# Optimization experiments

Hardware: AMD Instinct MI355X
Metric: run time of the kernel (lower is better)

## Reference

```python
import jax, jax.numpy as jnp
import numpy as np

SQRT_D_K = 64 ** 0.5  # d_model ** 0.5 from __init__
NEG_INF = -1e9


def setup_inputs() -> dict:
    key = jax.random.key(0)
    kq, kk, kv, kp = jax.random.split(key, 4)
    B, H, S, Dh = 4, 16, 2048, 64
    q = jax.random.normal(kq, (B, H, S, Dh), dtype=jnp.float32)
    k = jax.random.normal(kk, (B, H, S, Dh), dtype=jnp.float32)
    v = jax.random.normal(kv, (B, H, S, Dh), dtype=jnp.float32)
    # causal mask: 1 above the diagonal (positions to mask), [1,1,S,S]
    casual_mask = jnp.triu(jnp.ones((S, S), dtype=jnp.int32), k=1)[None, None]
    # padding mask: 1 marks padded tokens, [B,S]
    padding_mask = jax.random.randint(kp, (B, S), 0, 2, dtype=jnp.int32)
    return {"q": q, "k": k, "v": v, "casual_mask": casual_mask,
            "padding_mask": padding_mask}


def reference(q, k, v, casual_mask, padding_mask):
    # score: [B,H,S,S]
    score = jnp.einsum("bhqd,bhkd->bhqk", q, k) / SQRT_D_K
    score = jnp.where(casual_mask == 1, NEG_INF, score)
    score = jnp.where(padding_mask[:, None, None, :] == 1, NEG_INF, score)
    attn_weights = jax.nn.softmax(score, axis=-1)
    # dropout p=0.0 (eval) -> identity
    attention_output = jnp.einsum("bhqk,bhkd->bhqd", attn_weights, v)
    return attention_output, attn_weights
```

## Files before the change

### kernel.cpp

```cpp
#include <hip/hip_runtime.h>
#include <hip/hip_bf16.h>

#define S_LEN 2048
#define DH    64
#define QT    128
#define KT    64
#define NW    4

typedef __attribute__((ext_vector_type(8))) short bf16x8;
typedef __attribute__((ext_vector_type(4))) float f32x4;
typedef __attribute__((ext_vector_type(4))) unsigned u32x4;
typedef __attribute__((ext_vector_type(2))) unsigned u32x2;

static __device__ __forceinline__ unsigned cvtpk(float a, float b) {
    unsigned r;
    asm("v_cvt_pk_bf16_f32 %0, %1, %2" : "=v"(r) : "v"(a), "v"(b));
    return r;
}

__global__ __launch_bounds__(256) void attn_main(
    const float* __restrict__ Q, const float* __restrict__ K,
    const float* __restrict__ V, const int* __restrict__ PAD,
    float* __restrict__ OUT, float* __restrict__ W)
{
    __shared__ short Kt[KT][72];
    __shared__ short VT[DH][72];
    __shared__ short Pb[NW][16][72];
    __shared__ float sinv[2][NW][16];
    __shared__ unsigned long long padm[32];

    const int orig = blockIdx.x;
    const int wg   = (orig & 7) * 128 + (orig >> 3);
    const int bh   = wg >> 4;
    const int qt   = 15 - (wg & 15);
    const int b    = bh >> 4;
    const int q0   = qt * QT;

    const int tid  = threadIdx.x;
    const int wv   = tid >> 6;
    const int l    = tid & 63;
    const int lr   = l & 15;
    const int lg   = l >> 4;
    const int k2   = (tid & 31) * 2;
    const int dblk = (tid >> 5) * 8;

    const size_t hoff = (size_t)bh * S_LEN * DH;
    const float* Qh = Q + hoff;
    const float* Kh = K + hoff;
    const float* Vh = V + hoff;
    float* Oh = OUT + hoff;
    float* Wh = W + (size_t)bh * S_LEN * S_LEN;

    const int nkt    = 2 * qt + 2;
    const int ktmaxA = 2 * qt;

    for (int i = tid; i < S_LEN; i += 256) {
        unsigned long long m = __ballot(PAD[b * S_LEN + i] != 0);
        if (l == 0) padm[i >> 6] = m;
    }

    bf16x8 qfA[2], qfB[2];
    #pragma unroll
    for (int blk = 0; blk < 2; ++blk) {
        const float* qp = Qh + (size_t)(q0 + blk * 64 + wv * 16 + lr) * DH + lg * 8;
        #pragma unroll
        for (int h = 0; h < 2; ++h) {
            f32x4 a  = *reinterpret_cast<const f32x4*>(qp + h * 32);
            f32x4 b4 = *reinterpret_cast<const f32x4*>(qp + h * 32 + 4);
            u32x4 t;
            t[0] = cvtpk(a[0] * 0.125f,  a[1] * 0.125f);
            t[1] = cvtpk(a[2] * 0.125f,  a[3] * 0.125f);
            t[2] = cvtpk(b4[0] * 0.125f, b4[1] * 0.125f);
            t[3] = cvtpk(b4[2] * 0.125f, b4[3] * 0.125f);
            (blk ? qfB[h] : qfA[h]) = __builtin_bit_cast(bf16x8, t);
        }
    }

    const f32x4 z4 = {0.f, 0.f, 0.f, 0.f};
    f32x4 accA[4] = {z4, z4, z4, z4};
    f32x4 accB[4] = {z4, z4, z4, z4};
    float rsA = 0.f, rsB = 0.f;
    const int qcolA = q0 + wv * 16 + lr;
    const int qcolB = qcolA + 64;

    auto ablock = [&](const bf16x8 (&qf)[2], const int qcol, float& rsref,
                      f32x4 (&accb)[4], const unsigned long long pm, const int ktbase) {
        f32x4 sc[4] = {z4, z4, z4, z4};
        #pragma unroll
        for (int s = 0; s < 4; ++s)
            #pragma unroll
            for (int h = 0; h < 2; ++h) {
                bf16x8 kf = *reinterpret_cast<const bf16x8*>(&Kt[s * 16 + lr][h * 32 + lg * 8]);
                sc[s] = __builtin_amdgcn_mfma_f32_16x16x32_bf16(kf, qf[h], sc[s], 0, 0, 0);
            }
        #pragma unroll
        for (int s = 0; s < 4; ++s) {
            const int kbase = ktbase + s * 16 + lg * 4;
            float e[4];
            #pragma unroll
            for (int r = 0; r < 4; ++r) {
                const bool padded = (pm >> (s * 16 + lg * 4 + r)) & 1ull;
                const bool ok = (kbase + r <= qcol) && !padded;
                e[r] = ok ? __expf(sc[s][r]) : 0.f;
                rsref += e[r];
            }
            u32x2 p2 = { cvtpk(e[0], e[1]), cvtpk(e[2], e[3]) };
            *reinterpret_cast<u32x2*>(&Pb[wv][lr][s * 16 + lg * 4]) = p2;
        }
        #pragma unroll
        for (int kk = 0; kk < 2; ++kk) {
            bf16x8 pf = *reinterpret_cast<const bf16x8*>(&Pb[wv][lr][kk * 32 + lg * 8]);
            #pragma unroll
            for (int dt = 0; dt < 4; ++dt) {
                bf16x8 vf = *reinterpret_cast<const bf16x8*>(&VT[dt * 16 + lr][kk * 32 + lg * 8]);
                accb[dt] = __builtin_amdgcn_mfma_f32_16x16x32_bf16(pf, vf, accb[dt], 0, 0, 0);
            }
        }
    };

    for (int kt = 0; kt < nkt; ++kt) {
        __syncthreads();
        {
            const float* kp = Kh + ((size_t)(kt * KT) + l) * DH + wv * 16;
            f32x4 pk0 = *reinterpret_cast<const f32x4*>(kp);
            f32x4 pk1 = *reinterpret_cast<const f32x4*>(kp + 4);
            f32x4 pk2 = *reinterpret_cast<const f32x4*>(kp + 8);
            f32x4 pk3 = *reinterpret_cast<const f32x4*>(kp + 12);
            const float* vp = Vh + ((size_t)(kt * KT) + k2) * DH + dblk;
            f32x4 pva0 = *reinterpret_cast<const f32x4*>(vp);
            f32x4 pva1 = *reinterpret_cast<const f32x4*>(vp + 4);
            f32x4 pvb0 = *reinterpret_cast<const f32x4*>(vp + DH);
            f32x4 pvb1 = *reinterpret_cast<const f32x4*>(vp + DH + 4);
            u32x4 ta, tb;
            ta[0] = cvtpk(pk0[0], pk0[1]); ta[1] = cvtpk(pk0[2], pk0[3]);
            ta[2] = cvtpk(pk1[0], pk1[1]); ta[3] = cvtpk(pk1[2], pk1[3]);
            tb[0] = cvtpk(pk2[0], pk2[1]); tb[1] = cvtpk(pk2[2], pk2[3]);
            tb[2] = cvtpk(pk3[0], pk3[1]); tb[3] = cvtpk(pk3[2], pk3[3]);
            *reinterpret_cast<u32x4*>(&Kt[l][wv * 16])     = ta;
            *reinterpret_cast<u32x4*>(&Kt[l][wv * 16 + 8]) = tb;
            #pragma unroll
            for (int j = 0; j < 4; ++j)
                *reinterpret_cast<unsigned*>(&VT[dblk + j][k2])     = cvtpk(pva0[j], pvb0[j]);
            #pragma unroll
            for (int j = 0; j < 4; ++j)
                *reinterpret_cast<unsigned*>(&VT[dblk + 4 + j][k2]) = cvtpk(pva1[j], pvb1[j]);
        }
        __syncthreads();

        const unsigned long long pm = padm[kt];
        if (kt <= ktmaxA) ablock(qfA, qcolA, rsA, accA, pm, kt * KT);
        ablock(qfB, qcolB, rsB, accB, pm, kt * KT);
    }

    rsA += __shfl_xor(rsA, 16, 64); rsA += __shfl_xor(rsA, 32, 64);
    rsB += __shfl_xor(rsB, 16, 64); rsB += __shfl_xor(rsB, 32, 64);
    const float invA = rsA > 0.f ? 1.f / rsA : 0.f;
    const float invB = rsB > 0.f ? 1.f / rsB : 0.f;

    if (lg == 0) { sinv[0][wv][lr] = invA; sinv[1][wv][lr] = invB; }
    float inv4A[4], inv4B[4];
    #pragma unroll
    for (int r = 0; r < 4; ++r) {
        inv4A[r] = sinv[0][wv][lg * 4 + r];
        inv4B[r] = sinv[1][wv][lg * 4 + r];
    }

    const int qa = q0 + wv * 16 + lg * 4;
    #pragma unroll
    for (int dt = 0; dt < 4; ++dt)
        #pragma unroll
        for (int r = 0; r < 4; ++r) {
            Oh[(size_t)(qa + r) * DH + dt * 16 + lr]      = accA[dt][r] * inv4A[r];
            Oh[(size_t)(qa + 64 + r) * DH + dt * 16 + lr] = accB[dt][r] * inv4B[r];
        }

    auto wblock = [&](const bf16x8 (&qf)[2], const int qcol, const float inv,
                      const unsigned long long pm, const int ktbase) {
        f32x4 sc[4] = {z4, z4, z4, z4};
        #pragma unroll
        for (int s = 0; s < 4; ++s)
            #pragma unroll
            for (int h = 0; h < 2; ++h) {
                bf16x8 kf = *reinterpret_cast<const bf16x8*>(&Kt[s * 16 + lr][h * 32 + lg * 8]);
                sc[s] = __builtin_amdgcn_mfma_f32_16x16x32_bf16(kf, qf[h], sc[s], 0, 0, 0);
            }
        #pragma unroll
        for (int s = 0; s < 4; ++s) {
            const int kbase = ktbase + s * 16 + lg * 4;
            f32x4 t;
            #pragma unroll
            for (int r = 0; r < 4; ++r) {
                const bool padded = (pm >> (s * 16 + lg * 4 + r)) & 1ull;
                const bool ok = (kbase + r <= qcol) && !padded;
                t[r] = ok ? __expf(sc[s][r]) * inv : 0.f;
            }
            __builtin_nontemporal_store(t,
                reinterpret_cast<f32x4*>(Wh + (size_t)qcol * S_LEN + kbase));
        }
    };

    for (int kt = 0; kt < nkt; ++kt) {
        __syncthreads();
        {
            const float* kp = Kh + ((size_t)(kt * KT) + l) * DH + wv * 16;
            f32x4 pk0 = *reinterpret_cast<const f32x4*>(kp);
            f32x4 pk1 = *reinterpret_cast<const f32x4*>(kp + 4);
            f32x4 pk2 = *reinterpret_cast<const f32x4*>(kp + 8);
            f32x4 pk3 = *reinterpret_cast<const f32x4*>(kp + 12);
            u32x4 ta, tb;
            ta[0] = cvtpk(pk0[0], pk0[1]); ta[1] = cvtpk(pk0[2], pk0[3]);
            ta[2] = cvtpk(pk1[0], pk1[1]); ta[3] = cvtpk(pk1[2], pk1[3]);
            tb[0] = cvtpk(pk2[0], pk2[1]); tb[1] = cvtpk(pk2[2], pk2[3]);
            tb[2] = cvtpk(pk3[0], pk3[1]); tb[3] = cvtpk(pk3[2], pk3[3]);
            *reinterpret_cast<u32x4*>(&Kt[l][wv * 16])     = ta;
            *reinterpret_cast<u32x4*>(&Kt[l][wv * 16 + 8]) = tb;
        }
        __syncthreads();

        const unsigned long long pm = padm[kt];
        if (kt <= ktmaxA) wblock(qfA, qcolA, invA, pm, kt * KT);
        wblock(qfB, qcolB, invB, pm, kt * KT);
    }

    {
        #pragma unroll 1
        for (int row = 0; row < QT; ++row) {
            const int kend = q0 + (row < 64 ? 64 : 128);
            const int n4 = (S_LEN - kend) >> 2;
            f32x4* dst = reinterpret_cast<f32x4*>(Wh + (size_t)(q0 + row) * S_LEN + kend);
            for (int i = tid; i < n4; i += 256)
                __builtin_nontemporal_store(z4, dst + i);
        }
    }
}

__global__ __launch_bounds__(256) void attn_fixup(
    const int* __restrict__ PAD, const float* __restrict__ V,
    float* __restrict__ OUT, float* __restrict__ W)
{
    const int bh = blockIdx.x;
    const int b  = bh >> 4;
    const int tid = threadIdx.x;
    __shared__ int red;
    __shared__ float tmp[256];
    __shared__ float vs[DH];
    if (tid == 0) red = S_LEN;
    __syncthreads();
    int m = S_LEN;
    for (int i = tid; i < S_LEN; i += 256)
        if (PAD[b * S_LEN + i] == 0) m = min(m, i);
    atomicMin(&red, m);
    __syncthreads();
    const int fz = red;
    if (fz == 0) return;

    const float* Vh = V + (size_t)bh * S_LEN * DH;
    float a = 0.f;
    const int dcol = tid & 63, part = tid >> 6;
    for (int kk = part; kk < S_LEN; kk += 4) a += Vh[(size_t)kk * DH + dcol];
    tmp[tid] = a;
    __syncthreads();
    if (tid < DH)
        vs[tid] = (tmp[tid] + tmp[tid + 64] + tmp[tid + 128] + tmp[tid + 192]) * (1.f / S_LEN);
    __syncthreads();

    float* Wh = W + (size_t)bh * S_LEN * S_LEN;
    float* Oh = OUT + (size_t)bh * S_LEN * DH;
    const f32x4 u = {1.f / S_LEN, 1.f / S_LEN, 1.f / S_LEN, 1.f / S_LEN};
    for (int qa2 = 0; qa2 < fz; ++qa2) {
        f32x4* dst = reinterpret_cast<f32x4*>(Wh + (size_t)qa2 * S_LEN);
        for (int i = tid; i < S_LEN / 4; i += 256) dst[i] = u;
        if (tid < DH) Oh[(size_t)qa2 * DH + tid] = vs[tid];
    }
}

extern "C" void kernel_launch(void* const* d_in, const int* in_sizes, int n_in,
                              void* d_out, int out_size, void* d_ws, size_t ws_size,
                              hipStream_t stream) {
    const float* q   = (const float*)d_in[0];
    const float* k   = (const float*)d_in[1];
    const float* v   = (const float*)d_in[2];
    const int*   pad = (const int*)d_in[4];

    float* out = (float*)d_out;
    float* w   = out + (size_t)4 * 16 * S_LEN * DH;

    attn_main<<<dim3(64 * 16), dim3(256), 0, stream>>>(q, k, v, pad, out, w);
    attn_fixup<<<dim3(64), dim3(256), 0, stream>>>(pad, v, out, w);
}
```

Measured before the change: 472.7 us.

## Stage 128-key chunks per barrier and load K fragments directly into registers

Both passes now process two 64-key tiles per barrier pair: V (and, in the weight pass, K) for 128 keys is staged into a shared LDS pool, halving the number of __syncthreads. In the output pass, K fragments are loaded straight from global memory into registers per wave instead of going through LDS, and the LDS buffers are aliased inside one pool. This cuts barrier count and LDS traffic, but it duplicates K global loads across the four waves and raises register pressure, which could hurt occupancy.

```diff
diff --git a/kernel.cpp b/kernel.cpp
--- a/kernel.cpp
+++ b/kernel.cpp
@@ -23,11 +23,13 @@
     const float* __restrict__ V, const int* __restrict__ PAD,
     float* __restrict__ OUT, float* __restrict__ W)
 {
-    __shared__ short Kt[KT][72];
-    __shared__ short VT[DH][72];
-    __shared__ short Pb[NW][16][72];
+    __shared__ __align__(16) char pool[26624];
     __shared__ float sinv[2][NW][16];
     __shared__ unsigned long long padm[32];
+
+    short (*VT)[136]    = reinterpret_cast<short(*)[136]>(pool);
+    short (*Pb)[16][72] = reinterpret_cast<short(*)[16][72]>(pool + 17408);
+    short (*K2)[72]     = reinterpret_cast<short(*)[72]>(pool);
 
     const int orig = blockIdx.x;
     const int wg   = (orig & 7) * 128 + (orig >> 3);
@@ -51,7 +53,7 @@
     float* Oh = OUT + hoff;
     float* Wh = W + (size_t)bh * S_LEN * S_LEN;
 
-    const int nkt    = 2 * qt + 2;
+    const int NP     = qt + 1;
     const int ktmaxA = 2 * qt;
 
     for (int i = tid; i < S_LEN; i += 256) {
@@ -83,16 +85,32 @@
     const int qcolA = q0 + wv * 16 + lr;
     const int qcolB = qcolA + 64;
 
+    bf16x8 kfr[4][2];
+    auto loadK = [&](const int kt) {
+        #pragma unroll
+        for (int s = 0; s < 4; ++s) {
+            const float* kp = Kh + (size_t)(kt * KT + s * 16 + lr) * DH + lg * 8;
+            #pragma unroll
+            for (int h = 0; h < 2; ++h) {
+                f32x4 a  = *reinterpret_cast<const f32x4*>(kp + h * 32);
+                f32x4 b4 = *reinterpret_cast<const f32x4*>(kp + h * 32 + 4);
+                u32x4 t;
+                t[0] = cvtpk(a[0], a[1]);   t[1] = cvtpk(a[2], a[3]);
+                t[2] = cvtpk(b4[0], b4[1]); t[3] = cvtpk(b4[2], b4[3]);
+                kfr[s][h] = __builtin_bit_cast(bf16x8, t);
+            }
+        }
+    };
+
     auto ablock = [&](const bf16x8 (&qf)[2], const int qcol, float& rsref,
-                      f32x4 (&accb)[4], const unsigned long long pm, const int ktbase) {
+                      f32x4 (&accb)[4], const unsigned long long pm,
+                      const int ktbase, const int vtbase) {
         f32x4 sc[4] = {z4, z4, z4, z4};
         #pragma unroll
         for (int s = 0; s < 4; ++s)
             #pragma unroll
-            for (int h = 0; h < 2; ++h) {
-                bf16x8 kf = *reinterpret_cast<const bf16x8*>(&Kt[s * 16 + lr][h * 32 + lg * 8]);
-                sc[s] = __builtin_amdgcn_mfma_f32_16x16x32_bf16(kf, qf[h], sc[s], 0, 0, 0);
-            }
+            for (int h = 0; h < 2; ++h)
+                sc[s] = __builtin_amdgcn_mfma_f32_16x16x32_bf16(kfr[s][h], qf[h], sc[s], 0, 0, 0);
         #pragma unroll
         for (int s = 0; s < 4; ++s) {
             const int kbase = ktbase + s * 16 + lg * 4;
@@ -112,44 +130,44 @@
             bf16x8 pf = *reinterpret_cast<const bf16x8*>(&Pb[wv][lr][kk * 32 + lg * 8]);
             #pragma unroll
             for (int dt = 0; dt < 4; ++dt) {
-                bf16x8 vf = *reinterpret_cast<const bf16x8*>(&VT[dt * 16 + lr][kk * 32 + lg * 8]);
+                bf16x8 vf = *reinterpret_cast<const bf16x8*>(&VT[dt * 16 + lr][vtbase + kk * 32 + lg * 8]);
                 accb[dt] = __builtin_amdgcn_mfma_f32_16x16x32_bf16(pf, vf, accb[dt], 0, 0, 0);
             }
         }
     };
 
-    for (int kt = 0; kt < nkt; ++kt) {
+    for (int p = 0; p < NP; ++p) {
         __syncthreads();
         {
-            const float* kp = Kh + ((size_t)(kt * KT) + l) * DH + wv * 16;
-            f32x4 pk0 = *reinterpret_cast<const f32x4*>(kp);
-            f32x4 pk1 = *reinterpret_cast<const f32x4*>(kp + 4);
-            f32x4 pk2 = *reinterpret_cast<const f32x4*>(kp + 8);
-            f32x4 pk3 = *reinterpret_cast<const f32x4*>(kp + 12);
-            const float* vp = Vh + ((size_t)(kt * KT) + k2) * DH + dblk;
-            f32x4 pva0 = *reinterpret_cast<const f32x4*>(vp);
-            f32x4 pva1 = *reinterpret_cast<const f32x4*>(vp + 4);
-            f32x4 pvb0 = *reinterpret_cast<const f32x4*>(vp + DH);
-            f32x4 pvb1 = *reinterpret_cast<const f32x4*>(vp + DH + 4);
-            u32x4 ta, tb;
-            ta[0] = cvtpk(pk0[0], pk0[1]); ta[1] = cvtpk(pk0[2], pk0[3]);
-            ta[2] = cvtpk(pk1[0], pk1[1]); ta[3] = cvtpk(pk1[2], pk1[3]);
-            tb[0] = cvtpk(pk2[0], pk2[1]); tb[1] = cvtpk(pk2[2], pk2[3]);
-            tb[2] = cvtpk(pk3[0], pk3[1]); tb[3] = cvtpk(pk3[2], pk3[3]);
-            *reinterpret_cast<u32x4*>(&Kt[l][wv * 16])     = ta;
-            *reinterpret_cast<u32x4*>(&Kt[l][wv * 16 + 8]) = tb;
-            #pragma unroll
-            for (int j = 0; j < 4; ++j)
-                *reinterpret_cast<unsigned*>(&VT[dblk + j][k2])     = cvtpk(pva0[j], pvb0[j]);
-            #pragma unroll
-            for (int j = 0; j < 4; ++j)
-                *reinterpret_cast<unsigned*>(&VT[dblk + 4 + j][k2]) = cvtpk(pva1[j], pvb1[j]);
-        }
+            #pragma unroll
+            for (int h2 = 0; h2 < 2; ++h2) {
+                const float* vp = Vh + ((size_t)(p * 128 + h2 * 64) + k2) * DH + dblk;
+                f32x4 a0 = *reinterpret_cast<const f32x4*>(vp);
+                f32x4 a1 = *reinterpret_cast<const f32x4*>(vp + 4);
+                f32x4 b0 = *reinterpret_cast<const f32x4*>(vp + DH);
+                f32x4 b1 = *reinterpret_cast<const f32x4*>(vp + DH + 4);
+                #pragma unroll
+                for (int j = 0; j < 4; ++j)
+                    *reinterpret_cast<unsigned*>(&VT[dblk + j][h2 * 64 + k2])     = cvtpk(a0[j], b0[j]);
+                #pragma unroll
+                for (int j = 0; j < 4; ++j)
+                    *reinterpret_cast<unsigned*>(&VT[dblk + 4 + j][h2 * 64 + k2]) = cvtpk(a1[j], b1[j]);
+            }
+        }
+        loadK(2 * p);
         __syncthreads();
 
-        const unsigned long long pm = padm[kt];
-        if (kt <= ktmaxA) ablock(qfA, qcolA, rsA, accA, pm, kt * KT);
-        ablock(qfB, qcolB, rsB, accB, pm, kt * KT);
+        {
+            const unsigned long long pm = padm[2 * p];
+            if (2 * p <= ktmaxA) ablock(qfA, qcolA, rsA, accA, pm, 2 * p * KT, 0);
+            ablock(qfB, qcolB, rsB, accB, pm, 2 * p * KT, 0);
+        }
+        loadK(2 * p + 1);
+        {
+            const unsigned long long pm = padm[2 * p + 1];
+            if (2 * p + 1 <= ktmaxA) ablock(qfA, qcolA, rsA, accA, pm, (2 * p + 1) * KT, 64);
+            ablock(qfB, qcolB, rsB, accB, pm, (2 * p + 1) * KT, 64);
+        }
     }
 
     rsA += __shfl_xor(rsA, 16, 64); rsA += __shfl_xor(rsA, 32, 64);
@@ -175,13 +193,13 @@
         }
 
     auto wblock = [&](const bf16x8 (&qf)[2], const int qcol, const float inv,
-                      const unsigned long long pm, const int ktbase) {
+                      const unsigned long long pm, const int ktbase, const int trow) {
         f32x4 sc[4] = {z4, z4, z4, z4};
         #pragma unroll
         for (int s = 0; s < 4; ++s)
             #pragma unroll
             for (int h = 0; h < 2; ++h) {
-                bf16x8 kf = *reinterpret_cast<const bf16x8*>(&Kt[s * 16 + lr][h * 32 + lg * 8]);
+                bf16x8 kf = *reinterpret_cast<const bf16x8*>(&K2[trow + s * 16 + lr][h * 32 + lg * 8]);
                 sc[s] = __builtin_amdgcn_mfma_f32_16x16x32_bf16(kf, qf[h], sc[s], 0, 0, 0);
             }
         #pragma unroll
@@ -199,27 +217,35 @@
         }
     };
 
-    for (int kt = 0; kt < nkt; ++kt) {
+    for (int p = 0; p < NP; ++p) {
         __syncthreads();
         {
-            const float* kp = Kh + ((size_t)(kt * KT) + l) * DH + wv * 16;
-            f32x4 pk0 = *reinterpret_cast<const f32x4*>(kp);
-            f32x4 pk1 = *reinterpret_cast<const f32x4*>(kp + 4);
-            f32x4 pk2 = *reinterpret_cast<const f32x4*>(kp + 8);
-            f32x4 pk3 = *reinterpret_cast<const f32x4*>(kp + 12);
-            u32x4 ta, tb;
-            ta[0] = cvtpk(pk0[0], pk0[1]); ta[1] = cvtpk(pk0[2], pk0[3]);
-            ta[2] = cvtpk(pk1[0], pk1[1]); ta[3] = cvtpk(pk1[2], pk1[3]);
-            tb[0] = cvtpk(pk2[0], pk2[1]); tb[1] = cvtpk(pk2[2], pk2[3]);
-            tb[2] = cvtpk(pk3[0], pk3[1]); tb[3] = cvtpk(pk3[2], pk3[3]);
-            *reinterpret_cast<u32x4*>(&Kt[l][wv * 16])     = ta;
-            *reinterpret_cast<u32x4*>(&Kt[l][wv * 16 + 8]) = tb;
+            #pragma unroll
+            for (int h2 = 0; h2 < 2; ++h2) {
+                const int row = h2 * 64 + l;
+                const float* kp = Kh + (size_t)(p * 128 + row) * DH + wv * 16;
+                f32x4 k0 = *reinterpret_cast<const f32x4*>(kp);
+                f32x4 k1 = *reinterpret_cast<const f32x4*>(kp + 4);
+                f32x4 kx = *reinterpret_cast<const f32x4*>(kp + 8);
+                f32x4 k3 = *reinterpret_cast<const f32x4*>(kp + 12);
+                u32x4 ta, tb;
+                ta[0] = cvtpk(k0[0], k0[1]); ta[1] = cvtpk(k0[2], k0[3]);
+                ta[2] = cvtpk(k1[0], k1[1]); ta[3] = cvtpk(k1[2], k1[3]);
+                tb[0] = cvtpk(kx[0], kx[1]); tb[1] = cvtpk(kx[2], kx[3]);
+                tb[2] = cvtpk(k3[0], k3[1]); tb[3] = cvtpk(k3[2], k3[3]);
+                *reinterpret_cast<u32x4*>(&K2[row][wv * 16])     = ta;
+                *reinterpret_cast<u32x4*>(&K2[row][wv * 16 + 8]) = tb;
+            }
         }
         __syncthreads();
 
-        const unsigned long long pm = padm[kt];
-        if (kt <= ktmaxA) wblock(qfA, qcolA, invA, pm, kt * KT);
-        wblock(qfB, qcolB, invB, pm, kt * KT);
+        #pragma unroll
+        for (int t = 0; t < 2; ++t) {
+            const int kt = 2 * p + t;
+            const unsigned long long pm = padm[kt];
+            if (kt <= ktmaxA) wblock(qfA, qcolA, invA, pm, kt * KT, t * 64);
+            wblock(qfB, qcolB, invB, pm, kt * KT, t * 64);
+        }
     }
 
     {
```

New measurement: 544.8 us. +15.3%, slower.

## Pre-convert K and transposed V to bf16 in workspace before attention

Applied to the files above, without the earlier changes.

Adds a conversion kernel that packs K to bf16 and writes V transposed as bf16 into the workspace. The main attention kernel then loads ready-made bf16 tiles instead of converting fp32 K/V per tile in every query block. This removes repeated conversion and halves K/V read traffic across the 16 query tiles per head. The cost is one extra kernel launch plus the conversion pass, and the path falls back to the fp32 kernel when the workspace is too small.

```diff
diff --git a/kernel.cpp b/kernel.cpp
--- a/kernel.cpp
+++ b/kernel.cpp
@@ -18,7 +18,221 @@
     return r;
 }
 
-__global__ __launch_bounds__(256) void attn_main(
+#define KV_WORDS 4194304
+
+__global__ __launch_bounds__(256) void convert_kv(
+    const float* __restrict__ K, const float* __restrict__ V,
+    unsigned* __restrict__ Kb, unsigned* __restrict__ Vt)
+{
+    const int w = blockIdx.x * 256 + threadIdx.x;
+    {
+        const float2 v = reinterpret_cast<const float2*>(K)[w];
+        Kb[w] = cvtpk(v.x, v.y);
+    }
+    {
+        const int kw = w & 1023, d = (w >> 10) & 63, bh = w >> 16;
+        const float* vp = V + ((size_t)bh * S_LEN + kw * 2) * DH + d;
+        Vt[w] = cvtpk(vp[0], vp[DH]);
+    }
+}
+
+__global__ __launch_bounds__(256) void attn_main_bf16(
+    const float* __restrict__ Q, const unsigned* __restrict__ Kb,
+    const unsigned* __restrict__ Vt, const int* __restrict__ PAD,
+    float* __restrict__ OUT, float* __restrict__ W)
+{
+    __shared__ short Kt[KT][72];
+    __shared__ short VT[DH][72];
+    __shared__ short Pb[NW][16][72];
+    __shared__ float sinv[2][NW][16];
+    __shared__ unsigned long long padm[32];
+
+    const int orig = blockIdx.x;
+    const int wg   = (orig & 7) * 128 + (orig >> 3);
+    const int bh   = wg >> 4;
+    const int qt   = 15 - (wg & 15);
+    const int b    = bh >> 4;
+    const int q0   = qt * QT;
+
+    const int tid  = threadIdx.x;
+    const int wv   = tid >> 6;
+    const int l    = tid & 63;
+    const int lr   = l & 15;
+    const int lg   = l >> 4;
+    const int vd   = tid >> 2;
+    const int vp4  = tid & 3;
+
+    const size_t hoff = (size_t)bh * S_LEN * DH;
+    const float* Qh = Q + hoff;
+    const unsigned* Kbh = Kb + (size_t)bh * S_LEN * 32;
+    const unsigned* Vth = Vt + (size_t)bh * DH * 1024;
+    float* Oh = OUT + hoff;
+    float* Wh = W + (size_t)bh * S_LEN * S_LEN;
+
+    const int nkt    = 2 * qt + 2;
+    const int ktmaxA = 2 * qt;
+
+    for (int i = tid; i < S_LEN; i += 256) {
+        unsigned long long m = __ballot(PAD[b * S_LEN + i] != 0);
+        if (l == 0) padm[i >> 6] = m;
+    }
+
+    bf16x8 qfA[2], qfB[2];
+    #pragma unroll
+    for (int blk = 0; blk < 2; ++blk) {
+        const float* qp = Qh + (size_t)(q0 + blk * 64 + wv * 16 + lr) * DH + lg * 8;
+        #pragma unroll
+        for (int h = 0; h < 2; ++h) {
+            f32x4 a  = *reinterpret_cast<const f32x4*>(qp + h * 32);
+            f32x4 b4 = *reinterpret_cast<const f32x4*>(qp + h * 32 + 4);
+            u32x4 t;
+            t[0] = cvtpk(a[0] * 0.125f,  a[1] * 0.125f);
+            t[1] = cvtpk(a[2] * 0.125f,  a[3] * 0.125f);
+            t[2] = cvtpk(b4[0] * 0.125f, b4[1] * 0.125f);
+            t[3] = cvtpk(b4[2] * 0.125f, b4[3] * 0.125f);
+            (blk ? qfB[h] : qfA[h]) = __builtin_bit_cast(bf16x8, t);
+        }
+    }
+
+    const f32x4 z4 = {0.f, 0.f, 0.f, 0.f};
+    f32x4 accA[4] = {z4, z4, z4, z4};
+    f32x4 accB[4] = {z4, z4, z4, z4};
+    float rsA = 0.f, rsB = 0.f;
+    const int qcolA = q0 + wv * 16 + lr;
+    const int qcolB = qcolA + 64;
+
+    auto ablock = [&](const bf16x8 (&qf)[2], const int qcol, float& rsref,
+                      f32x4 (&accb)[4], const unsigned long long pm, const int ktbase) {
+        f32x4 sc[4] = {z4, z4, z4, z4};
+        #pragma unroll
+        for (int s = 0; s < 4; ++s)
+            #pragma unroll
+            for (int h = 0; h < 2; ++h) {
+                bf16x8 kf = *reinterpret_cast<const bf16x8*>(&Kt[s * 16 + lr][h * 32 + lg * 8]);
+                sc[s] = __builtin_amdgcn_mfma_f32_16x16x32_bf16(kf, qf[h], sc[s], 0, 0, 0);
+            }
+        #pragma unroll
+        for (int s = 0; s < 4; ++s) {
+            const int kbase = ktbase + s * 16 + lg * 4;
+            float e[4];
+            #pragma unroll
+            for (int r = 0; r < 4; ++r) {
+                const bool padded = (pm >> (s * 16 + lg * 4 + r)) & 1ull;
+                const bool ok = (kbase + r <= qcol) && !padded;
+                e[r] = ok ? __expf(sc[s][r]) : 0.f;
+                rsref += e[r];
+            }
+            u32x2 p2 = { cvtpk(e[0], e[1]), cvtpk(e[2], e[3]) };
+            *reinterpret_cast<u32x2*>(&Pb[wv][lr][s * 16 + lg * 4]) = p2;
+        }
+        #pragma unroll
+        for (int kk = 0; kk < 2; ++kk) {
+            bf16x8 pf = *reinterpret_cast<const bf16x8*>(&Pb[wv][lr][kk * 32 + lg * 8]);
+            #pragma unroll
+            for (int dt = 0; dt < 4; ++dt) {
+                bf16x8 vf = *reinterpret_cast<const bf16x8*>(&VT[dt * 16 + lr][kk * 32 + lg * 8]);
+                accb[dt] = __builtin_amdgcn_mfma_f32_16x16x32_bf16(pf, vf, accb[dt], 0, 0, 0);
+            }
+        }
+    };
+
+    for (int kt = 0; kt < nkt; ++kt) {
+        __syncthreads();
+        {
+            const unsigned* kb = Kbh + (size_t)(kt * KT + l) * 32 + wv * 8;
+            u32x4 a0 = *reinterpret_cast<const u32x4*>(kb);
+            u32x4 a1 = *reinterpret_cast<const u32x4*>(kb + 4);
+            *reinterpret_cast<u32x4*>(&Kt[l][wv * 16])     = a0;
+            *reinterpret_cast<u32x4*>(&Kt[l][wv * 16 + 8]) = a1;
+            const unsigned* vt = Vth + (size_t)vd * 1024 + kt * 32 + vp4 * 8;
+            u32x4 v0 = *reinterpret_cast<const u32x4*>(vt);
+            u32x4 v1 = *reinterpret_cast<const u32x4*>(vt + 4);
+            *reinterpret_cast<u32x4*>(&VT[vd][vp4 * 16])     = v0;
+            *reinterpret_cast<u32x4*>(&VT[vd][vp4 * 16 + 8]) = v1;
+        }
+        __syncthreads();
+
+        const unsigned long long pm = padm[kt];
+        if (kt <= ktmaxA) ablock(qfA, qcolA, rsA, accA, pm, kt * KT);
+        ablock(qfB, qcolB, rsB, accB, pm, kt * KT);
+    }
+
+    rsA += __shfl_xor(rsA, 16, 64); rsA += __shfl_xor(rsA, 32, 64);
+    rsB += __shfl_xor(rsB, 16, 64); rsB += __shfl_xor(rsB, 32, 64);
+    const float invA = rsA > 0.f ? 1.f / rsA : 0.f;
+    const float invB = rsB > 0.f ? 1.f / rsB : 0.f;
+
+    if (lg == 0) { sinv[0][wv][lr] = invA; sinv[1][wv][lr] = invB; }
+    float inv4A[4], inv4B[4];
+    #pragma unroll
+    for (int r = 0; r < 4; ++r) {
+        inv4A[r] = sinv[0][wv][lg * 4 + r];
+        inv4B[r] = sinv[1][wv][lg * 4 + r];
+    }
+
+    const int qa = q0 + wv * 16 + lg * 4;
+    #pragma unroll
+    for (int dt = 0; dt < 4; ++dt)
+        #pragma unroll
+        for (int r = 0; r < 4; ++r) {
+            Oh[(size_t)(qa + r) * DH + dt * 16 + lr]      = accA[dt][r] * inv4A[r];
+            Oh[(size_t)(qa + 64 + r) * DH + dt * 16 + lr] = accB[dt][r] * inv4B[r];
+        }
+
+    auto wblock = [&](const bf16x8 (&qf)[2], const int qcol, const float inv,
+                      const unsigned long long pm, const int ktbase) {
+        f32x4 sc[4] = {z4, z4, z4, z4};
+        #pragma unroll
+        for (int s = 0; s < 4; ++s)
+            #pragma unroll
+            for (int h = 0; h < 2; ++h) {
+                bf16x8 kf = *reinterpret_cast<const bf16x8*>(&Kt[s * 16 + lr][h * 32 + lg * 8]);
+                sc[s] = __builtin_amdgcn_mfma_f32_16x16x32_bf16(kf, qf[h], sc[s], 0, 0, 0);
+            }
+        #pragma unroll
+        for (int s = 0; s < 4; ++s) {
+            const int kbase = ktbase + s * 16 + lg * 4;
+            f32x4 t;
+            #pragma unroll
+            for (int r = 0; r < 4; ++r) {
+                const bool padded = (pm >> (s * 16 + lg * 4 + r)) & 1ull;
+                const bool ok = (kbase + r <= qcol) && !padded;
+                t[r] = ok ? __expf(sc[s][r]) * inv : 0.f;
+            }
+            __builtin_nontemporal_store(t,
+                reinterpret_cast<f32x4*>(Wh + (size_t)qcol * S_LEN + kbase));
+        }
+    };
+
+    for (int kt = 0; kt < nkt; ++kt) {
+        __syncthreads();
+        {
+            const unsigned* kb = Kbh + (size_t)(kt * KT + l) * 32 + wv * 8;
+            u32x4 a0 = *reinterpret_cast<const u32x4*>(kb);
+            u32x4 a1 = *reinterpret_cast<const u32x4*>(kb + 4);
+            *reinterpret_cast<u32x4*>(&Kt[l][wv * 16])     = a0;
+            *reinterpret_cast<u32x4*>(&Kt[l][wv * 16 + 8]) = a1;
+        }
+        __syncthreads();
+
+        const unsigned long long pm = padm[kt];
+        if (kt <= ktmaxA) wblock(qfA, qcolA, invA, pm, kt * KT);
+        wblock(qfB, qcolB, invB, pm, kt * KT);
+    }
+
+    {
+        #pragma unroll 1
+        for (int row = 0; row < QT; ++row) {
+            const int kend = q0 + (row < 64 ? 64 : 128);
+            const int n4 = (S_LEN - kend) >> 2;
+            f32x4* dst = reinterpret_cast<f32x4*>(Wh + (size_t)(q0 + row) * S_LEN + kend);
+            for (int i = tid; i < n4; i += 256)
+                __builtin_nontemporal_store(z4, dst + i);
+        }
+    }
+}
+
+__global__ __launch_bounds__(256) void attn_main_f32(
     const float* __restrict__ Q, const float* __restrict__ K,
     const float* __restrict__ V, const int* __restrict__ PAD,
     float* __restrict__ OUT, float* __restrict__ W)
@@ -285,6 +499,13 @@
     float* out = (float*)d_out;
     float* w   = out + (size_t)4 * 16 * S_LEN * DH;
 
-    attn_main<<<dim3(64 * 16), dim3(256), 0, stream>>>(q, k, v, pad, out, w);
+    if (ws_size >= (size_t)2 * KV_WORDS * 4) {
+        unsigned* kb = (unsigned*)d_ws;
+        unsigned* vt = kb + KV_WORDS;
+        convert_kv<<<dim3(KV_WORDS / 256), dim3(256), 0, stream>>>(k, v, kb, vt);
+        attn_main_bf16<<<dim3(64 * 16), dim3(256), 0, stream>>>(q, kb, vt, pad, out, w);
+    } else {
+        attn_main_f32<<<dim3(64 * 16), dim3(256), 0, stream>>>(q, k, v, pad, out, w);
+    }
     attn_fixup<<<dim3(64), dim3(256), 0, stream>>>(pad, v, out, w);
 }
```

New measurement: 507.4 us. 1.07x slower.

## Use persistent atomic-ticket scheduler with 64-row query tiles for causal attention

Applied to the files above, without the earlier changes.

Replaces the fixed grid of 128-row query tiles (each block handling two 64-row halves) with 64-row work items, dispatched longest-first through a global atomic ticket counter by a persistent grid of 1024 blocks. The goal is to balance the triangular causal workload across CUs and shrink the tail caused by uneven tile costs. In exchange, K/V tiles are no longer shared between two query halves, so K/V global loads and bf16 conversions are duplicated. It also adds a memset, a per-item atomic, and an extra barrier.

```diff
diff --git a/kernel.cpp b/kernel.cpp
--- a/kernel.cpp
+++ b/kernel.cpp
@@ -1,11 +1,11 @@
 #include <hip/hip_runtime.h>
 #include <hip/hip_bf16.h>
 
-#define S_LEN 2048
-#define DH    64
-#define QT    128
-#define KT    64
-#define NW    4
+#define S_LEN  2048
+#define DH     64
+#define KT     64
+#define NW     4
+#define NITEMS 2048
 
 typedef __attribute__((ext_vector_type(8))) short bf16x8;
 typedef __attribute__((ext_vector_type(4))) float f32x4;
@@ -18,23 +18,18 @@
     return r;
 }
 
-__global__ __launch_bounds__(256) void attn_main(
+template<bool TICKET>
+__global__ __launch_bounds__(256) void attn_persist(
     const float* __restrict__ Q, const float* __restrict__ K,
     const float* __restrict__ V, const int* __restrict__ PAD,
-    float* __restrict__ OUT, float* __restrict__ W)
+    float* __restrict__ OUT, float* __restrict__ W, unsigned* counter)
 {
     __shared__ short Kt[KT][72];
     __shared__ short VT[DH][72];
     __shared__ short Pb[NW][16][72];
-    __shared__ float sinv[2][NW][16];
+    __shared__ float sinv[NW][16];
     __shared__ unsigned long long padm[32];
-
-    const int orig = blockIdx.x;
-    const int wg   = (orig & 7) * 128 + (orig >> 3);
-    const int bh   = wg >> 4;
-    const int qt   = 15 - (wg & 15);
-    const int b    = bh >> 4;
-    const int q0   = qt * QT;
+    __shared__ unsigned sticket;
 
     const int tid  = threadIdx.x;
     const int wv   = tid >> 6;
@@ -43,194 +38,190 @@
     const int lg   = l >> 4;
     const int k2   = (tid & 31) * 2;
     const int dblk = (tid >> 5) * 8;
-
-    const size_t hoff = (size_t)bh * S_LEN * DH;
-    const float* Qh = Q + hoff;
-    const float* Kh = K + hoff;
-    const float* Vh = V + hoff;
-    float* Oh = OUT + hoff;
-    float* Wh = W + (size_t)bh * S_LEN * S_LEN;
-
-    const int nkt    = 2 * qt + 2;
-    const int ktmaxA = 2 * qt;
-
-    for (int i = tid; i < S_LEN; i += 256) {
-        unsigned long long m = __ballot(PAD[b * S_LEN + i] != 0);
-        if (l == 0) padm[i >> 6] = m;
-    }
-
-    bf16x8 qfA[2], qfB[2];
-    #pragma unroll
-    for (int blk = 0; blk < 2; ++blk) {
-        const float* qp = Qh + (size_t)(q0 + blk * 64 + wv * 16 + lr) * DH + lg * 8;
+    const f32x4 z4 = {0.f, 0.f, 0.f, 0.f};
+
+    for (;;) {
+        unsigned item;
+        if (TICKET) {
+            if (tid == 0) sticket = atomicAdd(counter, 1u);
+            __syncthreads();
+            item = sticket;
+            if (item >= NITEMS) return;
+        } else {
+            item = blockIdx.x;
+        }
+
+        const int qt  = 31 - (int)(item >> 6);
+        const int bh  = item & 63;
+        const int b   = bh >> 4;
+        const int q0  = qt * 64;
+        const int nkt = qt + 1;
+
+        const size_t hoff = (size_t)bh * S_LEN * DH;
+        const float* Qh = Q + hoff;
+        const float* Kh = K + hoff;
+        const float* Vh = V + hoff;
+        float* Oh = OUT + hoff;
+        float* Wh = W + (size_t)bh * S_LEN * S_LEN;
+
+        for (int i = tid; i < S_LEN; i += 256) {
+            unsigned long long m = __ballot(PAD[b * S_LEN + i] != 0);
+            if (l == 0) padm[i >> 6] = m;
+        }
+
+        bf16x8 qf[2];
+        {
+            const float* qp = Qh + (size_t)(q0 + wv * 16 + lr) * DH + lg * 8;
+            #pragma unroll
+            for (int h = 0; h < 2; ++h) {
+                f32x4 a  = *reinterpret_cast<const f32x4*>(qp + h * 32);
+                f32x4 b4 = *reinterpret_cast<const f32x4*>(qp + h * 32 + 4);
+                u32x4 t;
+                t[0] = cvtpk(a[0] * 0.125f,  a[1] * 0.125f);
+                t[1] = cvtpk(a[2] * 0.125f,  a[3] * 0.125f);
+                t[2] = cvtpk(b4[0] * 0.125f, b4[1] * 0.125f);
+                t[3] = cvtpk(b4[2] * 0.125f, b4[3] * 0.125f);
+                qf[h] = __builtin_bit_cast(bf16x8, t);
+            }
+        }
+
+        f32x4 acc[4] = {z4, z4, z4, z4};
+        float rs = 0.f;
+        const int qcol = q0 + wv * 16 + lr;
+
+        for (int kt = 0; kt < nkt; ++kt) {
+            __syncthreads();
+            {
+                const float* kp = Kh + ((size_t)(kt * KT) + l) * DH + wv * 16;
+                f32x4 pk0 = *reinterpret_cast<const f32x4*>(kp);
+                f32x4 pk1 = *reinterpret_cast<const f32x4*>(kp + 4);
+                f32x4 pk2 = *reinterpret_cast<const f32x4*>(kp + 8);
+                f32x4 pk3 = *reinterpret_cast<const f32x4*>(kp + 12);
+                const float* vp = Vh + ((size_t)(kt * KT) + k2) * DH + dblk;
+                f32x4 pva0 = *reinterpret_cast<const f32x4*>(vp);
+                f32x4 pva1 = *reinterpret_cast<const f32x4*>(vp + 4);
+                f32x4 pvb0 = *reinterpret_cast<const f32x4*>(vp + DH);
+                f32x4 pvb1 = *reinterpret_cast<const f32x4*>(vp + DH + 4);
+                u32x4 ta, tb;
+                ta[0] = cvtpk(pk0[0], pk0[1]); ta[1] = cvtpk(pk0[2], pk0[3]);
+                ta[2] = cvtpk(pk1[0], pk1[1]); ta[3] = cvtpk(pk1[2], pk1[3]);
+                tb[0] = cvtpk(pk2[0], pk2[1]); tb[1] = cvtpk(pk2[2], pk2[3]);
+                tb[2] = cvtpk(pk3[0], pk3[1]); tb[3] = cvtpk(pk3[2], pk3[3]);
+                *reinterpret_cast<u32x4*>(&Kt[l][wv * 16])     = ta;
+                *reinterpret_cast<u32x4*>(&Kt[l][wv * 16 + 8]) = tb;
+                #pragma unroll
+                for (int j = 0; j < 4; ++j)
+                    *reinterpret_cast<unsigned*>(&VT[dblk + j][k2])     = cvtpk(pva0[j], pvb0[j]);
+                #pragma unroll
+                for (int j = 0; j < 4; ++j)
+                    *reinterpret_cast<unsigned*>(&VT[dblk + 4 + j][k2]) = cvtpk(pva1[j], pvb1[j]);
+            }
+            __syncthreads();
+
+            const unsigned long long pm = padm[kt];
+            f32x4 sc[4] = {z4, z4, z4, z4};
+            #pragma unroll
+            for (int s = 0; s < 4; ++s)
+                #pragma unroll
+                for (int h = 0; h < 2; ++h) {
+                    bf16x8 kf = *reinterpret_cast<const bf16x8*>(&Kt[s * 16 + lr][h * 32 + lg * 8]);
+                    sc[s] = __builtin_amdgcn_mfma_f32_16x16x32_bf16(kf, qf[h], sc[s], 0, 0, 0);
+                }
+            #pragma unroll
+            for (int s = 0; s < 4; ++s) {
+                const int kbase = kt * KT + s * 16 + lg * 4;
+                float e[4];
+                #pragma unroll
+                for (int r = 0; r < 4; ++r) {
+                    const bool padded = (pm >> (s * 16 + lg * 4 + r)) & 1ull;
+                    const bool ok = (kbase + r <= qcol) && !padded;
+                    e[r] = ok ? __expf(sc[s][r]) : 0.f;
+                    rs += e[r];
+                }
+                u32x2 p2 = { cvtpk(e[0], e[1]), cvtpk(e[2], e[3]) };
+                *reinterpret_cast<u32x2*>(&Pb[wv][lr][s * 16 + lg * 4]) = p2;
+            }
+            #pragma unroll
+            for (int kk = 0; kk < 2; ++kk) {
+                bf16x8 pf = *reinterpret_cast<const bf16x8*>(&Pb[wv][lr][kk * 32 + lg * 8]);
+                #pragma unroll
+                for (int dt = 0; dt < 4; ++dt) {
+                    bf16x8 vf = *reinterpret_cast<const bf16x8*>(&VT[dt * 16 + lr][kk * 32 + lg * 8]);
+                    acc[dt] = __builtin_amdgcn_mfma_f32_16x16x32_bf16(pf, vf, acc[dt], 0, 0, 0);
+                }
+            }
+        }
+
+        rs += __shfl_xor(rs, 16, 64);
+        rs += __shfl_xor(rs, 32, 64);
+        const float inv = rs > 0.f ? 1.f / rs : 0.f;
+
+        if (lg == 0) sinv[wv][lr] = inv;
+        float inv4[4];
         #pragma unroll
-        for (int h = 0; h < 2; ++h) {
-            f32x4 a  = *reinterpret_cast<const f32x4*>(qp + h * 32);
-            f32x4 b4 = *reinterpret_cast<const f32x4*>(qp + h * 32 + 4);
-            u32x4 t;
-            t[0] = cvtpk(a[0] * 0.125f,  a[1] * 0.125f);
-            t[1] = cvtpk(a[2] * 0.125f,  a[3] * 0.125f);
-            t[2] = cvtpk(b4[0] * 0.125f, b4[1] * 0.125f);
-            t[3] = cvtpk(b4[2] * 0.125f, b4[3] * 0.125f);
-            (blk ? qfB[h] : qfA[h]) = __builtin_bit_cast(bf16x8, t);
-        }
-    }
-
-    const f32x4 z4 = {0.f, 0.f, 0.f, 0.f};
-    f32x4 accA[4] = {z4, z4, z4, z4};
-    f32x4 accB[4] = {z4, z4, z4, z4};
-    float rsA = 0.f, rsB = 0.f;
-    const int qcolA = q0 + wv * 16 + lr;
-    const int qcolB = qcolA + 64;
-
-    auto ablock = [&](const bf16x8 (&qf)[2], const int qcol, float& rsref,
-                      f32x4 (&accb)[4], const unsigned long long pm, const int ktbase) {
-        f32x4 sc[4] = {z4, z4, z4, z4};
+        for (int r = 0; r < 4; ++r) inv4[r] = sinv[wv][lg * 4 + r];
+
+        const int qa = q0 + wv * 16 + lg * 4;
         #pragma unroll
-        for (int s = 0; s < 4; ++s)
-            #pragma unroll
-            for (int h = 0; h < 2; ++h) {
-                bf16x8 kf = *reinterpret_cast<const bf16x8*>(&Kt[s * 16 + lr][h * 32 + lg * 8]);
-                sc[s] = __builtin_amdgcn_mfma_f32_16x16x32_bf16(kf, qf[h], sc[s], 0, 0, 0);
-            }
-        #pragma unroll
-        for (int s = 0; s < 4; ++s) {
-            const int kbase = ktbase + s * 16 + lg * 4;
-            float e[4];
-            #pragma unroll
-            for (int r = 0; r < 4; ++r) {
-                const bool padded = (pm >> (s * 16 + lg * 4 + r)) & 1ull;
-                const bool ok = (kbase + r <= qcol) && !padded;
-                e[r] = ok ? __expf(sc[s][r]) : 0.f;
-                rsref += e[r];
-            }
-            u32x2 p2 = { cvtpk(e[0], e[1]), cvtpk(e[2], e[3]) };
-            *reinterpret_cast<u32x2*>(&Pb[wv][lr][s * 16 + lg * 4]) = p2;
-        }
-        #pragma unroll
-        for (int kk = 0; kk < 2; ++kk) {
-            bf16x8 pf = *reinterpret_cast<const bf16x8*>(&Pb[wv][lr][kk * 32 + lg * 8]);
-            #pragma unroll
-            for (int dt = 0; dt < 4; ++dt) {
-                bf16x8 vf = *reinterpret_cast<const bf16x8*>(&VT[dt * 16 + lr][kk * 32 + lg * 8]);
-                accb[dt] = __builtin_amdgcn_mfma_f32_16x16x32_bf16(pf, vf, accb[dt], 0, 0, 0);
-            }
-        }
-    };
-
-    for (int kt = 0; kt < nkt; ++kt) {
-        __syncthreads();
+        for (int dt = 0; dt < 4; ++dt)
+            #pragma unroll
+            for (int r = 0; r < 4; ++r)
+                Oh[(size_t)(qa + r) * DH + dt * 16 + lr] = acc[dt][r] * inv4[r];
+
+        for (int kt = 0; kt < nkt; ++kt) {
+            __syncthreads();
+            {
+                const float* kp = Kh + ((size_t)(kt * KT) + l) * DH + wv * 16;
+                f32x4 pk0 = *reinterpret_cast<const f32x4*>(kp);
+                f32x4 pk1 = *reinterpret_cast<const f32x4*>(kp + 4);
+                f32x4 pk2 = *reinterpret_cast<const f32x4*>(kp + 8);
+                f32x4 pk3 = *reinterpret_cast<const f32x4*>(kp + 12);
+                u32x4 ta, tb;
+                ta[0] = cvtpk(pk0[0], pk0[1]); ta[1] = cvtpk(pk0[2], pk0[3]);
+                ta[2] = cvtpk(pk1[0], pk1[1]); ta[3] = cvtpk(pk1[2], pk1[3]);
+                tb[0] = cvtpk(pk2[0], pk2[1]); tb[1] = cvtpk(pk2[2], pk2[3]);
+                tb[2] = cvtpk(pk3[0], pk3[1]); tb[3] = cvtpk(pk3[2], pk3[3]);
+                *reinterpret_cast<u32x4*>(&Kt[l][wv * 16])     = ta;
+                *reinterpret_cast<u32x4*>(&Kt[l][wv * 16 + 8]) = tb;
+            }
+            __syncthreads();
+
+            const unsigned long long pm = padm[kt];
+            f32x4 sc[4] = {z4, z4, z4, z4};
+            #pragma unroll
+            for (int s = 0; s < 4; ++s)
+                #pragma unroll
+                for (int h = 0; h < 2; ++h) {
+                    bf16x8 kf = *reinterpret_cast<const bf16x8*>(&Kt[s * 16 + lr][h * 32 + lg * 8]);
+                    sc[s] = __builtin_amdgcn_mfma_f32_16x16x32_bf16(kf, qf[h], sc[s], 0, 0, 0);
+                }
+            #pragma unroll
+            for (int s = 0; s < 4; ++s) {
+                const int kbase = kt * KT + s * 16 + lg * 4;
+                f32x4 t;
+                #pragma unroll
+                for (int r = 0; r < 4; ++r) {
+                    const bool padded = (pm >> (s * 16 + lg * 4 + r)) & 1ull;
+                    const bool ok = (kbase + r <= qcol) && !padded;
+                    t[r] = ok ? __expf(sc[s][r]) * inv : 0.f;
+                }
+                __builtin_nontemporal_store(t,
+                    reinterpret_cast<f32x4*>(Wh + (size_t)qcol * S_LEN + kbase));
+            }
+        }
+
         {
-            const float* kp = Kh + ((size_t)(kt * KT) + l) * DH + wv * 16;
-            f32x4 pk0 = *reinterpret_cast<const f32x4*>(kp);
-            f32x4 pk1 = *reinterpret_cast<const f32x4*>(kp + 4);
-            f32x4 pk2 = *reinterpret_cast<const f32x4*>(kp + 8);
-            f32x4 pk3 = *reinterpret_cast<const f32x4*>(kp + 12);
-            const float* vp = Vh + ((size_t)(kt * KT) + k2) * DH + dblk;
-            f32x4 pva0 = *reinterpret_cast<const f32x4*>(vp);
-            f32x4 pva1 = *reinterpret_cast<const f32x4*>(vp + 4);
-            f32x4 pvb0 = *reinterpret_cast<const f32x4*>(vp + DH);
-            f32x4 pvb1 = *reinterpret_cast<const f32x4*>(vp + DH + 4);
-            u32x4 ta, tb;
-            ta[0] = cvtpk(pk0[0], pk0[1]); ta[1] = cvtpk(pk0[2], pk0[3]);
-            ta[2] = cvtpk(pk1[0], pk1[1]); ta[3] = cvtpk(pk1[2], pk1[3]);
-            tb[0] = cvtpk(pk2[0], pk2[1]); tb[1] = cvtpk(pk2[2], pk2[3]);
-            tb[2] = cvtpk(pk3[0], pk3[1]); tb[3] = cvtpk(pk3[2], pk3[3]);
-            *reinterpret_cast<u32x4*>(&Kt[l][wv * 16])     = ta;
-            *reinterpret_cast<u32x4*>(&Kt[l][wv * 16 + 8]) = tb;
-            #pragma unroll
-            for (int j = 0; j < 4; ++j)
-                *reinterpret_cast<unsigned*>(&VT[dblk + j][k2])     = cvtpk(pva0[j], pvb0[j]);
-            #pragma unroll
-            for (int j = 0; j < 4; ++j)
-                *reinterpret_cast<unsigned*>(&VT[dblk + 4 + j][k2]) = cvtpk(pva1[j], pvb1[j]);
-        }
-        __syncthreads();
-
-        const unsigned long long pm = padm[kt];
-        if (kt <= ktmaxA) ablock(qfA, qcolA, rsA, accA, pm, kt * KT);
-        ablock(qfB, qcolB, rsB, accB, pm, kt * KT);
-    }
-
-    rsA += __shfl_xor(rsA, 16, 64); rsA += __shfl_xor(rsA, 32, 64);
-    rsB += __shfl_xor(rsB, 16, 64); rsB += __shfl_xor(rsB, 32, 64);
-    const float invA = rsA > 0.f ? 1.f / rsA : 0.f;
-    const float invB = rsB > 0.f ? 1.f / rsB : 0.f;
-
-    if (lg == 0) { sinv[0][wv][lr] = invA; sinv[1][wv][lr] = invB; }
-    float inv4A[4], inv4B[4];
-    #pragma unroll
-    for (int r = 0; r < 4; ++r) {
-        inv4A[r] = sinv[0][wv][lg * 4 + r];
-        inv4B[r] = sinv[1][wv][lg * 4 + r];
-    }
-
-    const int qa = q0 + wv * 16 + lg * 4;
-    #pragma unroll
-    for (int dt = 0; dt < 4; ++dt)
-        #pragma unroll
-        for (int r = 0; r < 4; ++r) {
-            Oh[(size_t)(qa + r) * DH + dt * 16 + lr]      = accA[dt][r] * inv4A[r];
-            Oh[(size_t)(qa + 64 + r) * DH + dt * 16 + lr] = accB[dt][r] * inv4B[r];
-        }
-
-    auto wblock = [&](const bf16x8 (&qf)[2], const int qcol, const float inv,
-                      const unsigned long long pm, const int ktbase) {
-        f32x4 sc[4] = {z4, z4, z4, z4};
-        #pragma unroll
-        for (int s = 0; s < 4; ++s)
-            #pragma unroll
-            for (int h = 0; h < 2; ++h) {
-                bf16x8 kf = *reinterpret_cast<const bf16x8*>(&Kt[s * 16 + lr][h * 32 + lg * 8]);
-                sc[s] = __builtin_amdgcn_mfma_f32_16x16x32_bf16(kf, qf[h], sc[s], 0, 0, 0);
-            }
-        #pragma unroll
-        for (int s = 0; s < 4; ++s) {
-            const int kbase = ktbase + s * 16 + lg * 4;
-            f32x4 t;
-            #pragma unroll
-            for (int r = 0; r < 4; ++r) {
-                const bool padded = (pm >> (s * 16 + lg * 4 + r)) & 1ull;
-                const bool ok = (kbase + r <= qcol) && !padded;
-                t[r] = ok ? __expf(sc[s][r]) * inv : 0.f;
-            }
-            __builtin_nontemporal_store(t,
-                reinterpret_cast<f32x4*>(Wh + (size_t)qcol * S_LEN + kbase));
-        }
-    };
-
-    for (int kt = 0; kt < nkt; ++kt) {
-        __syncthreads();
-        {
-            const float* kp = Kh + ((size_t)(kt * KT) + l) * DH + wv * 16;
-            f32x4 pk0 = *reinterpret_cast<const f32x4*>(kp);
-            f32x4 pk1 = *reinterpret_cast<const f32x4*>(kp + 4);
-            f32x4 pk2 = *reinterpret_cast<const f32x4*>(kp + 8);
-            f32x4 pk3 = *reinterpret_cast<const f32x4*>(kp + 12);
-            u32x4 ta, tb;
-            ta[0] = cvtpk(pk0[0], pk0[1]); ta[1] = cvtpk(pk0[2], pk0[3]);
-            ta[2] = cvtpk(pk1[0], pk1[1]); ta[3] = cvtpk(pk1[2], pk1[3]);
-            tb[0] = cvtpk(pk2[0], pk2[1]); tb[1] = cvtpk(pk2[2], pk2[3]);
-            tb[2] = cvtpk(pk3[0], pk3[1]); tb[3] = cvtpk(pk3[2], pk3[3]);
-            *reinterpret_cast<u32x4*>(&Kt[l][wv * 16])     = ta;
-            *reinterpret_cast<u32x4*>(&Kt[l][wv * 16 + 8]) = tb;
-        }
-        __syncthreads();
-
-        const unsigned long long pm = padm[kt];
-        if (kt <= ktmaxA) wblock(qfA, qcolA, invA, pm, kt * KT);
-        wblock(qfB, qcolB, invB, pm, kt * KT);
-    }
-
-    {
-        #pragma unroll 1
-        for (int row = 0; row < QT; ++row) {
-            const int kend = q0 + (row < 64 ? 64 : 128);
+            const int kend = q0 + 64;
             const int n4 = (S_LEN - kend) >> 2;
-            f32x4* dst = reinterpret_cast<f32x4*>(Wh + (size_t)(q0 + row) * S_LEN + kend);
-            for (int i = tid; i < n4; i += 256)
-                __builtin_nontemporal_store(z4, dst + i);
-        }
+            #pragma unroll 1
+            for (int row = 0; row < 64; ++row) {
+                f32x4* dst = reinterpret_cast<f32x4*>(Wh + (size_t)(q0 + row) * S_LEN + kend);
+                for (int i = tid; i < n4; i += 256)
+                    __builtin_nontemporal_store(z4, dst + i);
+            }
+        }
+
+        if (!TICKET) return;
     }
 }
 
@@ -285,6 +276,12 @@
     float* out = (float*)d_out;
     float* w   = out + (size_t)4 * 16 * S_LEN * DH;
 
-    attn_main<<<dim3(64 * 16), dim3(256), 0, stream>>>(q, k, v, pad, out, w);
+    if (ws_size >= 4) {
+        unsigned* counter = (unsigned*)d_ws;
+        hipMemsetAsync(counter, 0, 4, stream);
+        attn_persist<true><<<dim3(1024), dim3(256), 0, stream>>>(q, k, v, pad, out, w, counter);
+    } else {
+        attn_persist<false><<<dim3(NITEMS), dim3(256), 0, stream>>>(q, k, v, pad, out, w, nullptr);
+    }
     attn_fixup<<<dim3(64), dim3(256), 0, stream>>>(pad, v, out, w);
 }
```

Measured after the change: 546.1 us. 1.16x slower.
